# Performance work log

Hardware: AMD Instinct MI355X
Metric: run time of the kernel (lower is better)

Reference implementation:

```python
import jax, jax.numpy as jnp
import numpy as np
import math

B, N, IN_DIM, EMBED, HEADS = 1, 96, 128, 128, 4
HD = EMBED // HEADS  # head_dim = 32


def _layernorm(x, g, b, eps=1e-5):
    mu = jnp.mean(x, axis=-1, keepdims=True)
    var = jnp.var(x, axis=-1, keepdims=True)
    return (x - mu) * jax.lax.rsqrt(var + eps) * g + b


def setup_inputs() -> dict:
    key = jax.random.key(0)
    ks = jax.random.split(key, 3)
    x = jax.random.normal(ks[0], (B, N, N, IN_DIM), dtype=jnp.float32)
    W = jax.random.normal(ks[1], (IN_DIM, EMBED), dtype=jnp.float32) / math.sqrt(IN_DIM)
    b = jnp.zeros((EMBED,), jnp.float32)
    ln_g = jnp.ones((HD,), jnp.float32)
    ln_b = jnp.zeros((HD,), jnp.float32)
    Wf = jax.random.normal(ks[2], (IN_DIM + EMBED, EMBED), dtype=jnp.float32) / math.sqrt(IN_DIM + EMBED)
    bf = jnp.zeros((EMBED,), jnp.float32)
    ln2_g = jnp.ones((EMBED,), jnp.float32)
    ln2_b = jnp.zeros((EMBED,), jnp.float32)
    return {"x": x, "W": W, "b": b, "ln_g": ln_g, "ln_b": ln_b,
            "Wf": Wf, "bf": bf, "ln2_g": ln2_g, "ln2_b": ln2_b}


def reference(x, W, b, ln_g, ln_b, Wf, bf, ln2_g, ln2_b):
    # NOTE: original torch module shares ONE Linear across q/k/v1/v2 and ONE
    # LayerNorm across norms[0..2] (ModuleList([m]*k) aliases the module).
    Bq, Nq = x.shape[0], x.shape[1]
    p = (jnp.einsum('bxyi,ie->bxye', x, W) + b).reshape(Bq, Nq, Nq, HEADS, HD)
    pn = _layernorm(p, ln_g, ln_b)                         # q == k (shared params)
    scores = jnp.einsum('bxahd,bayhd->bxayh', pn, pn) / math.sqrt(HD)
    att = jax.nn.softmax(scores, axis=2)                   # softmax over a
    x_upd = jnp.einsum('bxahd,bayhd->bxayhd', p, p)        # v1 == v2 == p
    x_upd = _layernorm(x_upd, ln_g, ln_b)                  # shared norm params
    agg = jnp.einsum('bxayh,bxayhd->bxyhd', att, x_upd).reshape(Bq, Nq, Nq, EMBED)
    cat = jnp.concatenate([x, agg], axis=-1)
    out = jnp.einsum('bxyc,ce->bxye', cat, Wf) + bf
    return _layernorm(out, ln2_g, ln2_b)
```

## Files before the change

### kernel.cpp

```cpp
#include <hip/hip_runtime.h>
#include <math.h>

#define NTOK 96
#define EMBED 128
#define HEADS 4
#define HD 32
#define NROW (NTOK*NTOK)
#define YT 16
#define NYT (NTOK/YT)

__global__ __launch_bounds__(128) void k_proj(
    const float* __restrict__ x, const float* __restrict__ W,
    const float* __restrict__ b,
    float* __restrict__ pT, float* __restrict__ murT) {
  const int r0 = blockIdx.x * 4;
  const int X  = r0 / NTOK;
  const int y0 = r0 % NTOK;
  const int e  = threadIdx.x;
  __shared__ float xt[EMBED][4];
  #pragma unroll
  for (int k = 0; k < 4; ++k)
    xt[e][k] = x[(size_t)(r0 + k) * EMBED + e];
  __syncthreads();

  const float bias = b[e];
  float a0 = bias, a1 = bias, a2 = bias, a3 = bias;
  #pragma unroll 8
  for (int i = 0; i < EMBED; ++i) {
    const float wv = W[(size_t)i * EMBED + e];
    const float4 c = *(const float4*)&xt[i][0];
    a0 = fmaf(wv, c.x, a0); a1 = fmaf(wv, c.y, a1);
    a2 = fmaf(wv, c.z, a2); a3 = fmaf(wv, c.w, a3);
  }

  const int h = e >> 5;
  float accs[4] = {a0, a1, a2, a3};
  #pragma unroll
  for (int k = 0; k < 4; ++k) {
    pT[((size_t)(y0 + k) * NTOK + X) * EMBED + e] = accs[k];
    float s1 = accs[k], s2 = accs[k] * accs[k];
    #pragma unroll
    for (int m_ = 1; m_ < 32; m_ <<= 1) {
      s1 += __shfl_xor(s1, m_, 64);
      s2 += __shfl_xor(s2, m_, 64);
    }
    if ((e & 31) == 0) {
      const float mu = s1 * (1.f / HD);
      const float var = fmaxf(s2 * (1.f / HD) - mu * mu, 0.f);
      float2 v; v.x = mu; v.y = rsqrtf(var + 1e-5f);
      *(float2*)&murT[(((size_t)(y0 + k) * NTOK + X) * HEADS + h) * 2] = v;
    }
  }
}

__device__ __forceinline__ void sc_elem(float e, float f, float g, float b,
    float rE, float pE, float rF, float pF,
    float& s, float& m, float& q, float& t) {
  const float uE = fmaf(e, rE, -pE);
  const float en = fmaf(uE, g, b);
  const float uF = fmaf(f, rF, -pF);
  const float fn = fmaf(uF, g, b);
  s = fmaf(en, fn, s);
  t = e * f;
  m += t;
  q = fmaf(t, t, q);
}

#define SC_QUAD(E4, F4, G4, B4, T4) \
  sc_elem(E4.x, F4.x, G4.x, B4.x, rE, pE, rF, pF, s, m, q, T4.x); \
  sc_elem(E4.y, F4.y, G4.y, B4.y, rE, pE, rF, pF, s, m, q, T4.y); \
  sc_elem(E4.z, F4.z, G4.z, B4.z, rE, pE, rF, pF, s, m, q, T4.z); \
  sc_elem(E4.w, F4.w, G4.w, B4.w, rE, pE, rF, pF, s, m, q, T4.w);

#define AGG_QUAD(A4, T4) \
  A4.x = fmaf(w, T4.x, A4.x); A4.y = fmaf(w, T4.y, A4.y); \
  A4.z = fmaf(w, T4.z, A4.z); A4.w = fmaf(w, T4.w, A4.w);

#define SCALE_QUAD(A4) \
  A4.x *= scale; A4.y *= scale; A4.z *= scale; A4.w *= scale;

#define RED_QUAD(A4, MASK) \
  A4.x += __shfl_xor(A4.x, MASK, 64); A4.y += __shfl_xor(A4.y, MASK, 64); \
  A4.z += __shfl_xor(A4.z, MASK, 64); A4.w += __shfl_xor(A4.w, MASK, 64);

__global__ __launch_bounds__(512) void k_fused(
    const float* __restrict__ pT, const float* __restrict__ murT,
    const float* __restrict__ ln_g, const float* __restrict__ ln_b,
    const float* __restrict__ x, const float* __restrict__ Wf,
    const float* __restrict__ bf, const float* __restrict__ g2,
    const float* __restrict__ b2, float* __restrict__ out) {
  const int bid = blockIdx.x;
  const int X   = bid % NTOK;
  const int y0  = (bid / NTOK) * YT;

  const int tid = threadIdx.x;
  const int hh  = tid >> 8;
  const int y   = (tid >> 4) & 15;
  const int ds  = (tid >> 3) & 1;
  const int da  = tid & 7;
  const int yy  = y0 + y;
  const int eoff = ds * 16;

  __shared__ float e_sm[2][NTOK][36];
  __shared__ float mur_sm[2][NTOK][2];
  __shared__ float xt_sm[EMBED][20];
  __shared__ float agg_t[EMBED][20];
  __shared__ float g_sm[HD], b_sm[HD];
  __shared__ float red_sm[8][4][2];

  #pragma unroll
  for (int i = 0; i < 4; ++i) {
    const int g = tid + i * 512;
    const int yl = g >> 7, col = g & 127;
    xt_sm[col][yl] = x[((size_t)(X * NTOK + y0 + yl)) * EMBED + col];
  }
  if (tid < HD) { g_sm[tid] = ln_g[tid]; b_sm[tid] = ln_b[tid]; }

  for (int hl = 0; hl < 2; ++hl) {
    __syncthreads();
    #pragma unroll
    for (int i = 0; i < 3; ++i) {
      const int g = tid + i * 512;
      const int h2 = g >> 9? (g >= 768 ? 1 : 1) : (g >= 768 ? 1 : 0);
      const int hd2 = (g >= 768) ? 1 : 0;
      const int rem = g - hd2 * 768;
      const int a = rem >> 3, qq = rem & 7;
      (void)h2;
      *(float4*)&e_sm[hd2][a][qq * 4] =
          *(const float4*)&pT[((size_t)a * NTOK + X) * EMBED + (hl * 2 + hd2) * HD + qq * 4];
    }
    if (tid < 192) {
      const int a = tid >> 1, h2s = tid & 1;
      *(float2*)&mur_sm[h2s][a][0] =
          *(const float2*)&murT[(((size_t)a * NTOK + X) * HEADS + hl * 2 + h2s) * 2];
    }
    __syncthreads();

    const int H = hl * 2 + hh;
    const float4 g0 = *(const float4*)&g_sm[eoff];
    const float4 g1 = *(const float4*)&g_sm[eoff + 4];
    const float4 g2v = *(const float4*)&g_sm[eoff + 8];
    const float4 g3 = *(const float4*)&g_sm[eoff + 12];
    const float4 b0 = *(const float4*)&b_sm[eoff];
    const float4 b1 = *(const float4*)&b_sm[eoff + 4];
    const float4 b2v = *(const float4*)&b_sm[eoff + 8];
    const float4 b3 = *(const float4*)&b_sm[eoff + 12];

    const float* fbase = pT + (size_t)yy * NTOK * EMBED + H * HD + eoff;
    const float* mbase = murT + ((size_t)yy * NTOK * HEADS + H) * 2;

    float4 acc0 = {0,0,0,0}, acc1 = {0,0,0,0}, acc2 = {0,0,0,0}, acc3 = {0,0,0,0};
    float den = 0.f, cc = 0.f, mx = -1e30f;

    #pragma unroll 2
    for (int ia = 0; ia < 12; ++ia) {
      const int a = ia * 8 + da;
      const float4* fp = (const float4*)(fbase + (size_t)a * EMBED);
      const float4 f0 = fp[0], f1 = fp[1], f2 = fp[2], f3 = fp[3];
      const float2 mrF = *(const float2*)(mbase + (size_t)a * (HEADS * 2));
      const float muE = mur_sm[hh][a][0], rE = mur_sm[hh][a][1];
      const float rF = mrF.y;
      const float pE = muE * rE;
      const float pF = mrF.x * rF;
      const float4 e0 = *(const float4*)&e_sm[hh][a][eoff];
      const float4 e1 = *(const float4*)&e_sm[hh][a][eoff + 4];
      const float4 e2 = *(const float4*)&e_sm[hh][a][eoff + 8];
      const float4 e3 = *(const float4*)&e_sm[hh][a][eoff + 12];

      float s = 0.f, m = 0.f, q = 0.f;
      float4 t0, t1, t2, t3;
      SC_QUAD(e0, f0, g0, b0, t0);
      SC_QUAD(e1, f1, g1, b1, t1);
      SC_QUAD(e2, f2, g2v, b2v, t2);
      SC_QUAD(e3, f3, g3, b3, t3);

      s += __shfl_xor(s, 8, 64);
      m += __shfl_xor(m, 8, 64);
      q += __shfl_xor(q, 8, 64);

      const float mu = m * (1.f / HD);
      const float var = fmaxf(fmaf(-mu, mu, q * (1.f / HD)), 0.f);
      const float r = rsqrtf(var + 1e-5f);
      const float sc = s * 0.17677669529663687f;

      float mc = sc;
      mc = fmaxf(mc, __shfl_xor(mc, 1, 64));
      mc = fmaxf(mc, __shfl_xor(mc, 2, 64));
      mc = fmaxf(mc, __shfl_xor(mc, 4, 64));
      const float nmx = fmaxf(mx, mc);
      const float scale = __expf(mx - nmx);
      mx = nmx;
      const float ex = __expf(sc - mx);
      const float w = ex * r;
      den = fmaf(den, scale, ex);
      cc  = fmaf(cc,  scale, w * mu);
      SCALE_QUAD(acc0); SCALE_QUAD(acc1); SCALE_QUAD(acc2); SCALE_QUAD(acc3);
      AGG_QUAD(acc0, t0);
      AGG_QUAD(acc1, t1);
      AGG_QUAD(acc2, t2);
      AGG_QUAD(acc3, t3);
    }

    #pragma unroll
    for (int mask = 1; mask <= 4; mask <<= 1) {
      den += __shfl_xor(den, mask, 64);
      cc  += __shfl_xor(cc,  mask, 64);
      RED_QUAD(acc0, mask);
      RED_QUAD(acc1, mask);
      RED_QUAD(acc2, mask);
      RED_QUAD(acc3, mask);
    }

    if (da == 0) {
      const float inv = 1.f / den;
      float ov[16];
      ov[0]  = fmaf(g0.x, (acc0.x - cc) * inv, b0.x);
      ov[1]  = fmaf(g0.y, (acc0.y - cc) * inv, b0.y);
      ov[2]  = fmaf(g0.z, (acc0.z - cc) * inv, b0.z);
      ov[3]  = fmaf(g0.w, (acc0.w - cc) * inv, b0.w);
      ov[4]  = fmaf(g1.x, (acc1.x - cc) * inv, b1.x);
      ov[5]  = fmaf(g1.y, (acc1.y - cc) * inv, b1.y);
      ov[6]  = fmaf(g1.z, (acc1.z - cc) * inv, b1.z);
      ov[7]  = fmaf(g1.w, (acc1.w - cc) * inv, b1.w);
      ov[8]  = fmaf(g2v.x, (acc2.x - cc) * inv, b2v.x);
      ov[9]  = fmaf(g2v.y, (acc2.y - cc) * inv, b2v.y);
      ov[10] = fmaf(g2v.z, (acc2.z - cc) * inv, b2v.z);
      ov[11] = fmaf(g2v.w, (acc2.w - cc) * inv, b2v.w);
      ov[12] = fmaf(g3.x, (acc3.x - cc) * inv, b3.x);
      ov[13] = fmaf(g3.y, (acc3.y - cc) * inv, b3.y);
      ov[14] = fmaf(g3.z, (acc3.z - cc) * inv, b3.z);
      ov[15] = fmaf(g3.w, (acc3.w - cc) * inv, b3.w);
      #pragma unroll
      for (int j = 0; j < 16; ++j)
        agg_t[H * HD + eoff + j][y] = ov[j];
    }
  }
  __syncthreads();

  const int e  = tid & 127;
  const int rh = tid >> 7;
  const float bias = bf[e];
  float acc4[4] = {bias, bias, bias, bias};

  #pragma unroll 8
  for (int i = 0; i < EMBED; ++i) {
    const float wv = Wf[(size_t)i * EMBED + e];
    const float4 c0 = *(const float4*)&xt_sm[i][rh * 4];
    acc4[0] = fmaf(wv, c0.x, acc4[0]); acc4[1] = fmaf(wv, c0.y, acc4[1]);
    acc4[2] = fmaf(wv, c0.z, acc4[2]); acc4[3] = fmaf(wv, c0.w, acc4[3]);
  }
  #pragma unroll 8
  for (int i = 0; i < EMBED; ++i) {
    const float wv = Wf[(size_t)(EMBED + i) * EMBED + e];
    const float4 c0 = *(const float4*)&agg_t[i][rh * 4];
    acc4[0] = fmaf(wv, c0.x, acc4[0]); acc4[1] = fmaf(wv, c0.y, acc4[1]);
    acc4[2] = fmaf(wv, c0.z, acc4[2]); acc4[3] = fmaf(wv, c0.w, acc4[3]);
  }

  const int wid = tid >> 6;
  #pragma unroll
  for (int k = 0; k < 4; ++k) {
    float s1 = acc4[k], s2 = acc4[k] * acc4[k];
    #pragma unroll
    for (int m_ = 1; m_ < 64; m_ <<= 1) {
      s1 += __shfl_xor(s1, m_, 64);
      s2 += __shfl_xor(s2, m_, 64);
    }
    if ((tid & 63) == 0) { red_sm[wid][k][0] = s1; red_sm[wid][k][1] = s2; }
  }
  __syncthreads();

  const float gg = g2[e], bb = b2[e];
  #pragma unroll
  for (int k = 0; k < 4; ++k) {
    const float S1 = red_sm[wid][k][0] + red_sm[wid ^ 1][k][0];
    const float S2 = red_sm[wid][k][1] + red_sm[wid ^ 1][k][1];
    const float mu = S1 * (1.f / EMBED);
    const float var = fmaxf(S2 * (1.f / EMBED) - mu * mu, 0.f);
    const float rstd = rsqrtf(var + 1e-5f);
    out[((size_t)(X * NTOK + y0 + rh * 4 + k)) * EMBED + e] =
        (acc4[k] - mu) * rstd * gg + bb;
  }
}

extern "C" void kernel_launch(void* const* d_in, const int* in_sizes, int n_in,
                              void* d_out, int out_size, void* d_ws, size_t ws_size,
                              hipStream_t stream) {
  const float* x    = (const float*)d_in[0];
  const float* W    = (const float*)d_in[1];
  const float* b    = (const float*)d_in[2];
  const float* ln_g = (const float*)d_in[3];
  const float* ln_b = (const float*)d_in[4];
  const float* Wf   = (const float*)d_in[5];
  const float* bf   = (const float*)d_in[6];
  const float* g2   = (const float*)d_in[7];
  const float* b2   = (const float*)d_in[8];
  float* out = (float*)d_out;

  float* pT   = (float*)d_ws;
  float* murT = pT + (size_t)NROW * EMBED;

  k_proj<<<NROW / 4, 128, 0, stream>>>(x, W, b, pT, murT);
  k_fused<<<NTOK * NYT, 512, 0, stream>>>(pT, murT, ln_g, ln_b,
                                          x, Wf, bf, g2, b2, out);
}
```

Measured before the change: 129.1 us.

## Restructure fused kernel to 8-row tiles with 16-way a-split per head

The fused attention kernel now handles 8 y-rows per block with 256 threads, looping over all four heads sequentially instead of two heads in parallel per half-block. The a-dimension is split 16 ways per lane group (6 iterations instead of 12), with wider shuffle reductions. This doubles the block count and halves shared memory per block, aiming for better occupancy and shorter serial loops on the 256-CU device, at the cost of more head-loop iterations, more syncs and more cross-lane reductions.

```diff
diff --git a/kernel.cpp b/kernel.cpp
--- a/kernel.cpp
+++ b/kernel.cpp
@@ -6,7 +6,7 @@
 #define HEADS 4
 #define HD 32
 #define NROW (NTOK*NTOK)
-#define YT 16
+#define YT 8
 #define NYT (NTOK/YT)
 
 __global__ __launch_bounds__(128) void k_proj(
@@ -83,7 +83,7 @@
   A4.x += __shfl_xor(A4.x, MASK, 64); A4.y += __shfl_xor(A4.y, MASK, 64); \
   A4.z += __shfl_xor(A4.z, MASK, 64); A4.w += __shfl_xor(A4.w, MASK, 64);
 
-__global__ __launch_bounds__(512) void k_fused(
+__global__ __launch_bounds__(256) void k_fused(
     const float* __restrict__ pT, const float* __restrict__ murT,
     const float* __restrict__ ln_g, const float* __restrict__ ln_b,
     const float* __restrict__ x, const float* __restrict__ Wf,
@@ -94,49 +94,42 @@
   const int y0  = (bid / NTOK) * YT;
 
   const int tid = threadIdx.x;
-  const int hh  = tid >> 8;
-  const int y   = (tid >> 4) & 15;
-  const int ds  = (tid >> 3) & 1;
-  const int da  = tid & 7;
+  const int y   = tid >> 5;
+  const int ds  = (tid >> 4) & 1;
+  const int da  = tid & 15;
   const int yy  = y0 + y;
   const int eoff = ds * 16;
 
-  __shared__ float e_sm[2][NTOK][36];
-  __shared__ float mur_sm[2][NTOK][2];
-  __shared__ float xt_sm[EMBED][20];
-  __shared__ float agg_t[EMBED][20];
+  __shared__ float e_sm[NTOK][36];
+  __shared__ float mur_sm[NTOK][2];
+  __shared__ float xt_sm[EMBED][12];
+  __shared__ float agg_t[EMBED][12];
   __shared__ float g_sm[HD], b_sm[HD];
-  __shared__ float red_sm[8][4][2];
+  __shared__ float red_sm[4][4][2];
 
   #pragma unroll
   for (int i = 0; i < 4; ++i) {
-    const int g = tid + i * 512;
+    const int g = tid + i * 256;
     const int yl = g >> 7, col = g & 127;
     xt_sm[col][yl] = x[((size_t)(X * NTOK + y0 + yl)) * EMBED + col];
   }
   if (tid < HD) { g_sm[tid] = ln_g[tid]; b_sm[tid] = ln_b[tid]; }
 
-  for (int hl = 0; hl < 2; ++hl) {
+  for (int H = 0; H < HEADS; ++H) {
     __syncthreads();
     #pragma unroll
     for (int i = 0; i < 3; ++i) {
-      const int g = tid + i * 512;
-      const int h2 = g >> 9? (g >= 768 ? 1 : 1) : (g >= 768 ? 1 : 0);
-      const int hd2 = (g >= 768) ? 1 : 0;
-      const int rem = g - hd2 * 768;
-      const int a = rem >> 3, qq = rem & 7;
-      (void)h2;
-      *(float4*)&e_sm[hd2][a][qq * 4] =
-          *(const float4*)&pT[((size_t)a * NTOK + X) * EMBED + (hl * 2 + hd2) * HD + qq * 4];
-    }
-    if (tid < 192) {
-      const int a = tid >> 1, h2s = tid & 1;
-      *(float2*)&mur_sm[h2s][a][0] =
-          *(const float2*)&murT[(((size_t)a * NTOK + X) * HEADS + hl * 2 + h2s) * 2];
+      const int g = tid + i * 256;
+      const int a = g >> 3, qq = g & 7;
+      *(float4*)&e_sm[a][qq * 4] =
+          *(const float4*)&pT[((size_t)a * NTOK + X) * EMBED + H * HD + qq * 4];
+    }
+    if (tid < NTOK) {
+      const float2 v = *(const float2*)&murT[(((size_t)tid * NTOK + X) * HEADS + H) * 2];
+      mur_sm[tid][0] = v.x; mur_sm[tid][1] = v.y;
     }
     __syncthreads();
 
-    const int H = hl * 2 + hh;
     const float4 g0 = *(const float4*)&g_sm[eoff];
     const float4 g1 = *(const float4*)&g_sm[eoff + 4];
     const float4 g2v = *(const float4*)&g_sm[eoff + 8];
@@ -153,19 +146,19 @@
     float den = 0.f, cc = 0.f, mx = -1e30f;
 
     #pragma unroll 2
-    for (int ia = 0; ia < 12; ++ia) {
-      const int a = ia * 8 + da;
+    for (int ia = 0; ia < 6; ++ia) {
+      const int a = ia * 16 + da;
       const float4* fp = (const float4*)(fbase + (size_t)a * EMBED);
       const float4 f0 = fp[0], f1 = fp[1], f2 = fp[2], f3 = fp[3];
       const float2 mrF = *(const float2*)(mbase + (size_t)a * (HEADS * 2));
-      const float muE = mur_sm[hh][a][0], rE = mur_sm[hh][a][1];
+      const float muE = mur_sm[a][0], rE = mur_sm[a][1];
       const float rF = mrF.y;
       const float pE = muE * rE;
       const float pF = mrF.x * rF;
-      const float4 e0 = *(const float4*)&e_sm[hh][a][eoff];
-      const float4 e1 = *(const float4*)&e_sm[hh][a][eoff + 4];
-      const float4 e2 = *(const float4*)&e_sm[hh][a][eoff + 8];
-      const float4 e3 = *(const float4*)&e_sm[hh][a][eoff + 12];
+      const float4 e0 = *(const float4*)&e_sm[a][eoff];
+      const float4 e1 = *(const float4*)&e_sm[a][eoff + 4];
+      const float4 e2 = *(const float4*)&e_sm[a][eoff + 8];
+      const float4 e3 = *(const float4*)&e_sm[a][eoff + 12];
 
       float s = 0.f, m = 0.f, q = 0.f;
       float4 t0, t1, t2, t3;
@@ -174,9 +167,9 @@
       SC_QUAD(e2, f2, g2v, b2v, t2);
       SC_QUAD(e3, f3, g3, b3, t3);
 
-      s += __shfl_xor(s, 8, 64);
-      m += __shfl_xor(m, 8, 64);
-      q += __shfl_xor(q, 8, 64);
+      s += __shfl_xor(s, 16, 64);
+      m += __shfl_xor(m, 16, 64);
+      q += __shfl_xor(q, 16, 64);
 
       const float mu = m * (1.f / HD);
       const float var = fmaxf(fmaf(-mu, mu, q * (1.f / HD)), 0.f);
@@ -187,6 +180,7 @@
       mc = fmaxf(mc, __shfl_xor(mc, 1, 64));
       mc = fmaxf(mc, __shfl_xor(mc, 2, 64));
       mc = fmaxf(mc, __shfl_xor(mc, 4, 64));
+      mc = fmaxf(mc, __shfl_xor(mc, 8, 64));
       const float nmx = fmaxf(mx, mc);
       const float scale = __expf(mx - nmx);
       mx = nmx;
@@ -202,7 +196,7 @@
     }
 
     #pragma unroll
-    for (int mask = 1; mask <= 4; mask <<= 1) {
+    for (int mask = 1; mask <= 8; mask <<= 1) {
       den += __shfl_xor(den, mask, 64);
       cc  += __shfl_xor(cc,  mask, 64);
       RED_QUAD(acc0, mask);
@@ -301,6 +295,6 @@
   float* murT = pT + (size_t)NROW * EMBED;
 
   k_proj<<<NROW / 4, 128, 0, stream>>>(x, W, b, pT, murT);
-  k_fused<<<NTOK * NYT, 512, 0, stream>>>(pT, murT, ln_g, ln_b,
+  k_fused<<<NTOK * NYT, 256, 0, stream>>>(pT, murT, ln_g, ln_b,
                                           x, Wf, bf, g2, b2, out);
 }
```

Measured after the change: 108.4 us. -16.0%, faster.
